# Performance work log

Hardware: AMD Instinct MI355X
Metric: run time of the kernel (lower is better)

The kernel has to match this reference:

```python
import jax, jax.numpy as jnp
import numpy as np

D_MODEL = 1024
NUM_HEADS = 16
HEAD_DIM = D_MODEL // NUM_HEADS
BATCH = 4
SEQ = 1024


def setup_inputs() -> dict:
    key = jax.random.key(0)
    ks = jax.random.split(key, 11)
    s = 1.0 / np.sqrt(D_MODEL)
    return {
        "query": jax.random.normal(ks[0], (BATCH, SEQ, D_MODEL), jnp.float32),
        "key_": jax.random.normal(ks[1], (BATCH, SEQ, D_MODEL), jnp.float32),
        "value": jax.random.normal(ks[2], (BATCH, SEQ, D_MODEL), jnp.float32),
        "Wq": jax.random.uniform(ks[3], (D_MODEL, D_MODEL), jnp.float32, -s, s),
        "bq": jax.random.uniform(ks[4], (D_MODEL,), jnp.float32, -s, s),
        "Wk": jax.random.uniform(ks[5], (D_MODEL, D_MODEL), jnp.float32, -s, s),
        "bk": jax.random.uniform(ks[6], (D_MODEL,), jnp.float32, -s, s),
        "Wv": jax.random.uniform(ks[7], (D_MODEL, D_MODEL), jnp.float32, -s, s),
        "bv": jax.random.uniform(ks[8], (D_MODEL,), jnp.float32, -s, s),
        "Wo": jax.random.uniform(ks[9], (D_MODEL, D_MODEL), jnp.float32, -s, s),
        "bo": jax.random.uniform(ks[10], (D_MODEL,), jnp.float32, -s, s),
    }


def reference(query, key_, value, Wq, bq, Wk, bk, Wv, bv, Wo, bo):
    B, S, _ = query.shape
    scale = 1.0 / np.sqrt(HEAD_DIM).astype(np.float32)
    # projections, then split heads: [B, H, S, Dh]
    Q = (query @ Wq.T + bq).reshape(B, S, NUM_HEADS, HEAD_DIM).transpose(0, 2, 1, 3)
    K = (key_ @ Wk.T + bk).reshape(B, S, NUM_HEADS, HEAD_DIM).transpose(0, 2, 1, 3)
    V = (value @ Wv.T + bv).reshape(B, S, NUM_HEADS, HEAD_DIM).transpose(0, 2, 1, 3)
    scores = jnp.einsum("bhqd,bhkd->bhqk", Q, K) * scale
    attention = jax.nn.softmax(scores, axis=-1)
    out = jnp.einsum("bhqk,bhkd->bhqd", attention, V)
    out = out.transpose(0, 2, 1, 3).reshape(B, S, D_MODEL)
    return out @ Wo.T + bo, attention
```

## Files before the change

kernel.cpp:

```cpp
#include <hip/hip_runtime.h>
#include <hip/hip_bf16.h>

#define NH 16
#define S 1024
#define DH 64
#define DM 1024
#define MTOK 4096

typedef __attribute__((ext_vector_type(8))) short bf16x8;
typedef __attribute__((ext_vector_type(4))) float f32x4;
typedef __attribute__((ext_vector_type(16))) float f32x16;
typedef __attribute__((ext_vector_type(8))) unsigned short u16x8;
typedef __attribute__((ext_vector_type(4))) unsigned short u16x4;

__device__ inline unsigned short f2bf(float x) {
  __hip_bfloat16 h = __float2bfloat16(x);
  return __builtin_bit_cast(unsigned short, h);
}

__device__ inline unsigned cvt_pk_bf16(float lo, float hi_) {
  unsigned r;
  asm("v_cvt_pk_bf16_f32 %0, %1, %2" : "=v"(r) : "v"(lo), "v"(hi_));
  return r;
}

__device__ inline void gload16(const void* g, void* lds) {
  __builtin_amdgcn_global_load_lds((const __attribute__((address_space(1))) void*)g,
                                   (__attribute__((address_space(3))) void*)lds, 16, 0, 0);
}

__global__ __launch_bounds__(256) void cvt_all(
    const float* __restrict__ q, const float* __restrict__ k, const float* __restrict__ v,
    const float* __restrict__ wq, const float* __restrict__ wk,
    const float* __restrict__ wv, const float* __restrict__ wo,
    unsigned short* __restrict__ xq, unsigned short* __restrict__ xk,
    unsigned short* __restrict__ xv, unsigned short* __restrict__ wqb,
    unsigned short* __restrict__ wkb, unsigned short* __restrict__ wvb,
    unsigned short* __restrict__ wob) {
  const int bid = blockIdx.x;
  const float* src;
  unsigned short* dst;
  int lb;
  if (bid < 6144) {
    const int r = bid >> 11;
    lb = bid & 2047;
    src = (r == 0) ? q : ((r == 1) ? k : v);
    dst = (r == 0) ? xq : ((r == 1) ? xk : xv);
  } else {
    const int r = (bid - 6144) >> 9;
    lb = (bid - 6144) & 511;
    src = (r == 0) ? wq : ((r == 1) ? wk : ((r == 2) ? wv : wo));
    dst = (r == 0) ? wqb : ((r == 1) ? wkb : ((r == 2) ? wvb : wob));
  }
  const int i = lb * 256 + threadIdx.x;
  const float4* s4 = (const float4*)(src + (size_t)i * 8);
  float4 v0 = s4[0], v1 = s4[1];
  u16x8 o;
  o[0] = f2bf(v0.x); o[1] = f2bf(v0.y); o[2] = f2bf(v0.z); o[3] = f2bf(v0.w);
  o[4] = f2bf(v1.x); o[5] = f2bf(v1.y); o[6] = f2bf(v1.z); o[7] = f2bf(v1.w);
  *(u16x8*)(dst + (size_t)i * 8) = o;
}

__device__ inline void gemm_core128(const unsigned short* __restrict__ X,
                                    const unsigned short* __restrict__ W,
                                    unsigned short* As, unsigned short* Bs,
                                    int m0, int n0, f32x4 acc[4][4]) {
  const int t = threadIdx.x, l = t & 63, w = t >> 6;
  const int wr = w >> 1, wc = w & 1, cl = l & 15, kg = l >> 4;
  const int row0 = w * 16 + (l >> 2);
  const int kcol = (l & 3) * 8;

  const unsigned short* ga0 = X + (size_t)(m0 + row0) * DM + kcol;
  const unsigned short* ga1 = ga0 + (size_t)64 * DM;
  const unsigned short* gb0 = W + (size_t)(n0 + row0) * DM + kcol;
  const unsigned short* gb1 = gb0 + (size_t)64 * DM;
  char* lA0 = (char*)As + w * 1024;
  char* lA1 = (char*)As + w * 1024 + 4096;
  char* lB0 = (char*)Bs + w * 1024;
  char* lB1 = (char*)Bs + w * 1024 + 4096;

  for (int kt = 0; kt < DM; kt += 32) {
    __syncthreads();
    gload16(ga0 + kt, lA0);
    gload16(ga1 + kt, lA1);
    gload16(gb0 + kt, lB0);
    gload16(gb1 + kt, lB1);
    __syncthreads();
    bf16x8 a[4], b[4];
#pragma unroll
    for (int m = 0; m < 4; ++m)
      a[m] = *(const bf16x8*)&As[(wr * 64 + m * 16 + cl) * 32 + kg * 8];
#pragma unroll
    for (int n = 0; n < 4; ++n)
      b[n] = *(const bf16x8*)&Bs[(wc * 64 + n * 16 + cl) * 32 + kg * 8];
#pragma unroll
    for (int m = 0; m < 4; ++m)
#pragma unroll
      for (int n = 0; n < 4; ++n)
        acc[m][n] = __builtin_amdgcn_mfma_f32_16x16x32_bf16(a[m], b[n], acc[m][n], 0, 0, 0);
  }
}

__global__ __launch_bounds__(256) void proj_gemm(
    const unsigned short* __restrict__ X0, const unsigned short* __restrict__ X1,
    const unsigned short* __restrict__ X2, const unsigned short* __restrict__ W0,
    const unsigned short* __restrict__ W1, const unsigned short* __restrict__ W2,
    const float* __restrict__ b0, const float* __restrict__ b1, const float* __restrict__ b2,
    unsigned short* __restrict__ Y0, unsigned short* __restrict__ Y1,
    unsigned short* __restrict__ Y2) {
  __shared__ unsigned short As[128 * 32];
  __shared__ unsigned short Bs[128 * 32];
  const int z = blockIdx.z;
  const unsigned short* X = (z == 0) ? X0 : ((z == 1) ? X1 : X2);
  const unsigned short* W = (z == 0) ? W0 : ((z == 1) ? W1 : W2);
  const float* bias = (z == 0) ? b0 : ((z == 1) ? b1 : b2);
  const int m0 = blockIdx.y * 128, n0 = blockIdx.x * 128;

  f32x4 acc[4][4] = {};
  gemm_core128(X, W, As, Bs, m0, n0, acc);

  const int l = threadIdx.x & 63, w = threadIdx.x >> 6;
  const int wr = w >> 1, wc = w & 1, cl = l & 15, kg = l >> 4;
#pragma unroll
  for (int i = 0; i < 4; ++i) {
#pragma unroll
    for (int j = 0; j < 4; ++j) {
      const int gn = n0 + wc * 64 + j * 16 + cl;
      const float bv = bias[gn];
      const int h_ = gn >> 6, d_ = gn & 63;
#pragma unroll
      for (int r = 0; r < 4; ++r) {
        const int gm = m0 + wr * 64 + i * 16 + kg * 4 + r;
        const int b_ = gm >> 10, s_ = gm & 1023;
        const float val = acc[i][j][r] + bv;
        if (z == 0) {
          Y0[((size_t)(b_ * NH + h_) * S + s_) * DH + d_] = f2bf(val);
        } else if (z == 1) {
          Y1[((size_t)(b_ * NH + h_) * S + s_) * DH + d_] = f2bf(val * 0.125f);
        } else {
          Y2[((size_t)(b_ * NH + h_) * DH + d_) * S + s_] = f2bf(val);
        }
      }
    }
  }
}

__global__ __launch_bounds__(256) void out_gemm(const unsigned short* __restrict__ X,
                                                const unsigned short* __restrict__ W,
                                                const float* __restrict__ bias,
                                                float* __restrict__ Y) {
  __shared__ unsigned short As[128 * 32];
  __shared__ unsigned short Bs[128 * 32];
  const int m0 = blockIdx.y * 128, n0 = blockIdx.x * 128;
  f32x4 acc[4][4] = {};
  gemm_core128(X, W, As, Bs, m0, n0, acc);
  const int l = threadIdx.x & 63, w = threadIdx.x >> 6;
  const int wr = w >> 1, wc = w & 1, cl = l & 15, kg = l >> 4;
#pragma unroll
  for (int i = 0; i < 4; ++i) {
#pragma unroll
    for (int j = 0; j < 4; ++j) {
      const int gn = n0 + wc * 64 + j * 16 + cl;
      const float bv = bias[gn];
#pragma unroll
      for (int r = 0; r < 4; ++r) {
        const int gm = m0 + wr * 64 + i * 16 + kg * 4 + r;
        Y[(size_t)gm * DM + gn] = acc[i][j][r] + bv;
      }
    }
  }
}

__global__ __launch_bounds__(512, 4) void attn_mfma(const unsigned short* __restrict__ Qh,
                                                    const unsigned short* __restrict__ Kh,
                                                    const unsigned short* __restrict__ Vt,
                                                    float* __restrict__ attn,
                                                    unsigned short* __restrict__ OutH) {
  __shared__ float sums[8][32];
  __shared__ float Olds[8 * 64 * 33];
  const int t = threadIdx.x, l = t & 63, w = t >> 6;
  const int lq = l & 31, hi = l >> 5;
  const int bh = blockIdx.y;
  const int q0 = blockIdx.x * 32;

  const unsigned short* kb = Kh + (size_t)bh * S * DH;
  const unsigned short* vb = Vt + (size_t)bh * DH * S;

  unsigned e_pk[4][8];
  float sum = 0.f;

  {
    const unsigned short* qp = Qh + ((size_t)bh * S + q0 + lq) * DH + hi * 8;
    bf16x8 qf0 = *(const bf16x8*)(qp);
    bf16x8 qf1 = *(const bf16x8*)(qp + 16);
    bf16x8 qf2 = *(const bf16x8*)(qp + 32);
    bf16x8 qf3 = *(const bf16x8*)(qp + 48);
#pragma unroll
    for (int kt = 0; kt < 4; ++kt) {
      const unsigned short* kp = kb + (size_t)(w * 128 + kt * 32 + lq) * DH + hi * 8;
      f32x16 acc = {};
      acc = __builtin_amdgcn_mfma_f32_32x32x16_bf16(*(const bf16x8*)(kp),      qf0, acc, 0, 0, 0);
      acc = __builtin_amdgcn_mfma_f32_32x32x16_bf16(*(const bf16x8*)(kp + 16), qf1, acc, 0, 0, 0);
      acc = __builtin_amdgcn_mfma_f32_32x32x16_bf16(*(const bf16x8*)(kp + 32), qf2, acc, 0, 0, 0);
      acc = __builtin_amdgcn_mfma_f32_32x32x16_bf16(*(const bf16x8*)(kp + 48), qf3, acc, 0, 0, 0);
      float e[16];
#pragma unroll
      for (int r = 0; r < 16; ++r) e[r] = __expf(acc[r]);
#pragma unroll
      for (int r = 0; r < 16; ++r) sum += e[r];
#pragma unroll
      for (int j = 0; j < 8; ++j) e_pk[kt][j] = cvt_pk_bf16(e[2 * j], e[2 * j + 1]);
    }
  }
  sum += __shfl_xor(sum, 32);
  if (l < 32) sums[w][lq] = sum;
  __syncthreads();
  float tot = 0.f;
#pragma unroll
  for (int p = 0; p < 8; ++p) tot += sums[p][lq];
  const float inv = 1.0f / tot;

  f32x16 o0 = {}, o1 = {};
  float* ab = attn + ((size_t)bh << 20) + ((size_t)(q0 + lq) << 10) + w * 128;

#pragma unroll
  for (int kt = 0; kt < 4; ++kt) {
#pragma unroll
    for (int g = 0; g < 4; ++g) {
      const unsigned pk0 = e_pk[kt][2 * g], pk1 = e_pk[kt][2 * g + 1];
      f32x4 pv;
      pv[0] = __builtin_bit_cast(float, pk0 << 16) * inv;
      pv[1] = __builtin_bit_cast(float, pk0 & 0xffff0000u) * inv;
      pv[2] = __builtin_bit_cast(float, pk1 << 16) * inv;
      pv[3] = __builtin_bit_cast(float, pk1 & 0xffff0000u) * inv;
      *(f32x4*)(ab + kt * 32 + 8 * g + 4 * hi) = pv;
    }

    const unsigned wds0 = e_pk[kt][0], wds1 = e_pk[kt][1];
    const unsigned wds2 = e_pk[kt][2], wds3 = e_pk[kt][3];
    const unsigned wds4 = e_pk[kt][4], wds5 = e_pk[kt][5];
    const unsigned wds6 = e_pk[kt][6], wds7 = e_pk[kt][7];
    const unsigned x0 = __shfl_xor((int)wds0, 32), x1 = __shfl_xor((int)wds1, 32);
    const unsigned x2 = __shfl_xor((int)wds2, 32), x3 = __shfl_xor((int)wds3, 32);
    const unsigned x4 = __shfl_xor((int)wds4, 32), x5 = __shfl_xor((int)wds5, 32);
    const unsigned x6 = __shfl_xor((int)wds6, 32), x7 = __shfl_xor((int)wds7, 32);
    union UU { unsigned u[4]; bf16x8 v; } f0, f1;
    f0.u[0] = hi ? x2 : wds0;  f0.u[1] = hi ? x3 : wds1;
    f0.u[2] = hi ? wds2 : x0;  f0.u[3] = hi ? wds3 : x1;
    f1.u[0] = hi ? x6 : wds4;  f1.u[1] = hi ? x7 : wds5;
    f1.u[2] = hi ? wds6 : x4;  f1.u[3] = hi ? wds7 : x5;

    {
      const unsigned short* vp = vb + (size_t)(lq)*S + w * 128 + kt * 32 + hi * 8;
      bf16x8 v0 = *(const bf16x8*)vp;
      bf16x8 v1 = *(const bf16x8*)(vp + 16);
      o0 = __builtin_amdgcn_mfma_f32_32x32x16_bf16(v0, f0.v, o0, 0, 0, 0);
      o0 = __builtin_amdgcn_mfma_f32_32x32x16_bf16(v1, f1.v, o0, 0, 0, 0);
    }
    {
      const unsigned short* vp = vb + (size_t)(32 + lq) * S + w * 128 + kt * 32 + hi * 8;
      bf16x8 v0 = *(const bf16x8*)vp;
      bf16x8 v1 = *(const bf16x8*)(vp + 16);
      o1 = __builtin_amdgcn_mfma_f32_32x32x16_bf16(v0, f0.v, o1, 0, 0, 0);
      o1 = __builtin_amdgcn_mfma_f32_32x32x16_bf16(v1, f1.v, o1, 0, 0, 0);
    }
  }

#pragma unroll
  for (int r = 0; r < 16; ++r) { o0[r] *= inv; o1[r] *= inv; }
#pragma unroll
  for (int g = 0; g < 4; ++g) {
#pragma unroll
    for (int r = 0; r < 4; ++r) {
      const int d = 8 * g + 4 * hi + r;
      Olds[w * 2112 + d * 33 + lq] = o0[4 * g + r];
      Olds[w * 2112 + (32 + d) * 33 + lq] = o1[4 * g + r];
    }
  }
  __syncthreads();

  if (t < 256) {
    const int qq = t >> 3, d0 = (t & 7) * 8;
    const int b_ = bh >> 4, h_ = bh & 15;
    u16x8 ov;
#pragma unroll
    for (int i = 0; i < 8; ++i) {
      float s = 0.f;
#pragma unroll
      for (int p = 0; p < 8; ++p) s += Olds[p * 2112 + (d0 + i) * 33 + qq];
      ov[i] = f2bf(s);
    }
    *(u16x8*)&OutH[((size_t)(b_ * S + q0 + qq)) * DM + h_ * DH + d0] = ov;
  }
}

extern "C" void kernel_launch(void* const* d_in, const int* in_sizes, int n_in,
                              void* d_out, int out_size, void* d_ws, size_t ws_size,
                              hipStream_t stream) {
  const float* query = (const float*)d_in[0];
  const float* key_  = (const float*)d_in[1];
  const float* value = (const float*)d_in[2];
  const float* Wq = (const float*)d_in[3];
  const float* bq = (const float*)d_in[4];
  const float* Wk = (const float*)d_in[5];
  const float* bk = (const float*)d_in[6];
  const float* Wv = (const float*)d_in[7];
  const float* bv = (const float*)d_in[8];
  const float* Wo = (const float*)d_in[9];
  const float* bo = (const float*)d_in[10];

  float* out0 = (float*)d_out;
  float* attn = out0 + (size_t)MTOK * DM;

  const size_t M1 = 1u << 20;
  unsigned short* wsu = (unsigned short*)d_ws;
  unsigned short* Xq  = wsu;
  unsigned short* Xk  = wsu + 4 * M1;
  unsigned short* Xv  = wsu + 8 * M1;
  unsigned short* Wqb = wsu + 12 * M1;
  unsigned short* Wkb = wsu + 13 * M1;
  unsigned short* Wvb = wsu + 14 * M1;
  unsigned short* Wob = wsu + 15 * M1;
  unsigned short* Qh  = wsu + 16 * M1;
  unsigned short* Kh  = wsu + 20 * M1;
  unsigned short* Vt  = wsu + 24 * M1;
  unsigned short* OutH= wsu + 28 * M1;

  dim3 tB(256);
  hipLaunchKernelGGL(cvt_all, dim3(8192), tB, 0, stream, query, key_, value, Wq, Wk, Wv, Wo,
                     Xq, Xk, Xv, Wqb, Wkb, Wvb, Wob);

  hipLaunchKernelGGL(proj_gemm, dim3(8, 32, 3), tB, 0, stream,
                     Xq, Xk, Xv, Wqb, Wkb, Wvb, bq, bk, bv, Qh, Kh, Vt);

  hipLaunchKernelGGL(attn_mfma, dim3(32, 64), dim3(512), 0, stream, Qh, Kh, Vt, attn, OutH);

  hipLaunchKernelGGL(out_gemm, dim3(8, 32), tB, 0, stream, OutH, Wob, bo, out0);
}
```

Before: 212.8 us.

## Shrink out-projection tile, vectorize V stores, add MFMA priority hints in attention

The output projection GEMM now uses 64x128 tiles, doubling the grid from 256 to 512 blocks to fill more compute units. The V-transpose store in the projection kernel writes four consecutive bf16 values as one vector instead of scalar stores. The attention kernel raises wave priority around its MFMA groups, loads both V fragments before issuing the PV MFMAs, and spreads the final head-sum reduction across all 512 threads instead of 256. The smaller GEMM tiles mean less data reuse per block and more redundant global loads.

```diff
diff --git a/kernel.cpp b/kernel.cpp
--- a/kernel.cpp
+++ b/kernel.cpp
@@ -101,6 +101,42 @@
   }
 }
 
+__device__ inline void gemm_core64(const unsigned short* __restrict__ X,
+                                   const unsigned short* __restrict__ W,
+                                   unsigned short* As, unsigned short* Bs,
+                                   int m0, int n0, f32x4 acc[2][4]) {
+  const int t = threadIdx.x, l = t & 63, w = t >> 6;
+  const int i4 = l >> 2, c8 = (l & 3) * 8;
+  const int wr = w >> 1, wc = w & 1, cl = l & 15, kg = l >> 4;
+
+  const unsigned short* ga  = X + (size_t)(m0 + w * 16 + i4) * DM + c8;
+  const unsigned short* gb0 = W + (size_t)(n0 + w * 32 + i4) * DM + c8;
+  const unsigned short* gb1 = W + (size_t)(n0 + w * 32 + 16 + i4) * DM + c8;
+  char* lA  = (char*)As + w * 1024;
+  char* lB0 = (char*)Bs + w * 2048;
+  char* lB1 = (char*)Bs + w * 2048 + 1024;
+
+  for (int kt = 0; kt < DM; kt += 32) {
+    __syncthreads();
+    gload16(ga + kt, lA);
+    gload16(gb0 + kt, lB0);
+    gload16(gb1 + kt, lB1);
+    __syncthreads();
+    bf16x8 a[2], b[4];
+#pragma unroll
+    for (int i = 0; i < 2; ++i)
+      a[i] = *(const bf16x8*)&As[(wr * 32 + i * 16 + cl) * 32 + kg * 8];
+#pragma unroll
+    for (int j = 0; j < 4; ++j)
+      b[j] = *(const bf16x8*)&Bs[(wc * 64 + j * 16 + cl) * 32 + kg * 8];
+#pragma unroll
+    for (int i = 0; i < 2; ++i)
+#pragma unroll
+      for (int j = 0; j < 4; ++j)
+        acc[i][j] = __builtin_amdgcn_mfma_f32_16x16x32_bf16(a[i], b[j], acc[i][j], 0, 0, 0);
+  }
+}
+
 __global__ __launch_bounds__(256) void proj_gemm(
     const unsigned short* __restrict__ X0, const unsigned short* __restrict__ X1,
     const unsigned short* __restrict__ X2, const unsigned short* __restrict__ W0,
@@ -128,17 +164,24 @@
       const int gn = n0 + wc * 64 + j * 16 + cl;
       const float bv = bias[gn];
       const int h_ = gn >> 6, d_ = gn & 63;
-#pragma unroll
-      for (int r = 0; r < 4; ++r) {
-        const int gm = m0 + wr * 64 + i * 16 + kg * 4 + r;
-        const int b_ = gm >> 10, s_ = gm & 1023;
-        const float val = acc[i][j][r] + bv;
-        if (z == 0) {
-          Y0[((size_t)(b_ * NH + h_) * S + s_) * DH + d_] = f2bf(val);
-        } else if (z == 1) {
-          Y1[((size_t)(b_ * NH + h_) * S + s_) * DH + d_] = f2bf(val * 0.125f);
-        } else {
-          Y2[((size_t)(b_ * NH + h_) * DH + d_) * S + s_] = f2bf(val);
+      if (z == 2) {
+        const int gm0 = m0 + wr * 64 + i * 16 + kg * 4;
+        const int b_ = gm0 >> 10, s0 = gm0 & 1023;
+        u16x4 vv;
+#pragma unroll
+        for (int r = 0; r < 4; ++r) vv[r] = f2bf(acc[i][j][r] + bv);
+        *(u16x4*)&Y2[((size_t)(b_ * NH + h_) * DH + d_) * S + s0] = vv;
+      } else {
+#pragma unroll
+        for (int r = 0; r < 4; ++r) {
+          const int gm = m0 + wr * 64 + i * 16 + kg * 4 + r;
+          const int b_ = gm >> 10, s_ = gm & 1023;
+          const float val = acc[i][j][r] + bv;
+          if (z == 0) {
+            Y0[((size_t)(b_ * NH + h_) * S + s_) * DH + d_] = f2bf(val);
+          } else {
+            Y1[((size_t)(b_ * NH + h_) * S + s_) * DH + d_] = f2bf(val * 0.125f);
+          }
         }
       }
     }
@@ -149,22 +192,22 @@
                                                 const unsigned short* __restrict__ W,
                                                 const float* __restrict__ bias,
                                                 float* __restrict__ Y) {
-  __shared__ unsigned short As[128 * 32];
+  __shared__ unsigned short As[64 * 32];
   __shared__ unsigned short Bs[128 * 32];
-  const int m0 = blockIdx.y * 128, n0 = blockIdx.x * 128;
-  f32x4 acc[4][4] = {};
-  gemm_core128(X, W, As, Bs, m0, n0, acc);
+  const int m0 = blockIdx.y * 64, n0 = blockIdx.x * 128;
+  f32x4 acc[2][4] = {};
+  gemm_core64(X, W, As, Bs, m0, n0, acc);
   const int l = threadIdx.x & 63, w = threadIdx.x >> 6;
   const int wr = w >> 1, wc = w & 1, cl = l & 15, kg = l >> 4;
 #pragma unroll
-  for (int i = 0; i < 4; ++i) {
+  for (int i = 0; i < 2; ++i) {
 #pragma unroll
     for (int j = 0; j < 4; ++j) {
       const int gn = n0 + wc * 64 + j * 16 + cl;
       const float bv = bias[gn];
 #pragma unroll
       for (int r = 0; r < 4; ++r) {
-        const int gm = m0 + wr * 64 + i * 16 + kg * 4 + r;
+        const int gm = m0 + wr * 32 + i * 16 + kg * 4 + r;
         Y[(size_t)gm * DM + gn] = acc[i][j][r] + bv;
       }
     }
@@ -199,10 +242,12 @@
     for (int kt = 0; kt < 4; ++kt) {
       const unsigned short* kp = kb + (size_t)(w * 128 + kt * 32 + lq) * DH + hi * 8;
       f32x16 acc = {};
+      __builtin_amdgcn_s_setprio(1);
       acc = __builtin_amdgcn_mfma_f32_32x32x16_bf16(*(const bf16x8*)(kp),      qf0, acc, 0, 0, 0);
       acc = __builtin_amdgcn_mfma_f32_32x32x16_bf16(*(const bf16x8*)(kp + 16), qf1, acc, 0, 0, 0);
       acc = __builtin_amdgcn_mfma_f32_32x32x16_bf16(*(const bf16x8*)(kp + 32), qf2, acc, 0, 0, 0);
       acc = __builtin_amdgcn_mfma_f32_32x32x16_bf16(*(const bf16x8*)(kp + 48), qf3, acc, 0, 0, 0);
+      __builtin_amdgcn_s_setprio(0);
       float e[16];
 #pragma unroll
       for (int r = 0; r < 16; ++r) e[r] = __expf(acc[r]);
@@ -254,15 +299,15 @@
       const unsigned short* vp = vb + (size_t)(lq)*S + w * 128 + kt * 32 + hi * 8;
       bf16x8 v0 = *(const bf16x8*)vp;
       bf16x8 v1 = *(const bf16x8*)(vp + 16);
+      const unsigned short* vp1 = vb + (size_t)(32 + lq) * S + w * 128 + kt * 32 + hi * 8;
+      bf16x8 v2 = *(const bf16x8*)vp1;
+      bf16x8 v3 = *(const bf16x8*)(vp1 + 16);
+      __builtin_amdgcn_s_setprio(1);
       o0 = __builtin_amdgcn_mfma_f32_32x32x16_bf16(v0, f0.v, o0, 0, 0, 0);
       o0 = __builtin_amdgcn_mfma_f32_32x32x16_bf16(v1, f1.v, o0, 0, 0, 0);
-    }
-    {
-      const unsigned short* vp = vb + (size_t)(32 + lq) * S + w * 128 + kt * 32 + hi * 8;
-      bf16x8 v0 = *(const bf16x8*)vp;
-      bf16x8 v1 = *(const bf16x8*)(vp + 16);
-      o1 = __builtin_amdgcn_mfma_f32_32x32x16_bf16(v0, f0.v, o1, 0, 0, 0);
-      o1 = __builtin_amdgcn_mfma_f32_32x32x16_bf16(v1, f1.v, o1, 0, 0, 0);
+      o1 = __builtin_amdgcn_mfma_f32_32x32x16_bf16(v2, f0.v, o1, 0, 0, 0);
+      o1 = __builtin_amdgcn_mfma_f32_32x32x16_bf16(v3, f1.v, o1, 0, 0, 0);
+      __builtin_amdgcn_s_setprio(0);
     }
   }
 
@@ -279,18 +324,18 @@
   }
   __syncthreads();
 
-  if (t < 256) {
-    const int qq = t >> 3, d0 = (t & 7) * 8;
+  {
+    const int qq = t >> 4, d0 = (t & 15) * 4;
     const int b_ = bh >> 4, h_ = bh & 15;
-    u16x8 ov;
-#pragma unroll
-    for (int i = 0; i < 8; ++i) {
+    u16x4 ov;
+#pragma unroll
+    for (int i = 0; i < 4; ++i) {
       float s = 0.f;
 #pragma unroll
       for (int p = 0; p < 8; ++p) s += Olds[p * 2112 + (d0 + i) * 33 + qq];
       ov[i] = f2bf(s);
     }
-    *(u16x8*)&OutH[((size_t)(b_ * S + q0 + qq)) * DM + h_ * DH + d0] = ov;
+    *(u16x4*)&OutH[((size_t)(b_ * S + q0 + qq)) * DM + h_ * DH + d0] = ov;
   }
 }
 
@@ -335,5 +380,5 @@
 
   hipLaunchKernelGGL(attn_mfma, dim3(32, 64), dim3(512), 0, stream, Qh, Kh, Vt, attn, OutH);
 
-  hipLaunchKernelGGL(out_gemm, dim3(8, 32), tB, 0, stream, OutH, Wob, bo, out0);
-}
+  hipLaunchKernelGGL(out_gemm, dim3(8, 64), tB, 0, stream, OutH, Wob, bo, out0);
+}
```

Result: faster. 199.7 us (-6.1%).
